# Performance work log

Hardware: AMD Instinct MI355X
Metric: run time of the kernel (lower is better)

The kernel has to match this reference:

```python
import jax, jax.numpy as jnp
import numpy as np

N_NODES = 50000
N_EDGES = 1600000
D = 128        # fea_dim == hidden_units == dim_z
L = 3          # num_layers


def _gin_params(key, scale=0.05):
    ks = jax.random.split(key, 7)
    return dict(
        W1=jax.random.normal(ks[0], (L, D, D), jnp.float32) * scale,
        b1=jnp.zeros((L, D), jnp.float32),
        W2=jax.random.normal(ks[1], (L, D, D), jnp.float32) * scale,
        b2=jnp.zeros((L, D), jnp.float32),
        eps=jnp.zeros((L,), jnp.float32),
        Wout=jax.random.normal(ks[2], (D, D), jnp.float32) * scale,
        bout=jnp.zeros((D,), jnp.float32),
    )


def setup_inputs() -> dict:
    key = jax.random.key(0)
    k_x, k_s, k_d, k_m, k_sd = jax.random.split(key, 5)
    inp = {
        'x': jax.random.normal(k_x, (N_NODES, D), jnp.float32),
        'edge_src': jax.random.randint(k_s, (N_EDGES,), 0, N_NODES, jnp.int32),
        'edge_dst': jax.random.randint(k_d, (N_EDGES,), 0, N_NODES, jnp.int32),
    }
    for pref, k in (('mean_', k_m), ('std_', k_sd)):
        for name, v in _gin_params(k).items():
            inp[pref + name] = v
    inp['ln_gamma'] = jnp.ones((D,), jnp.float32)
    inp['ln_beta'] = jnp.zeros((D,), jnp.float32)
    return inp


def _gin(x, src, dst, W1, b1, W2, b2, eps, Wout, bout):
    # Standard GIN: h = MLP((1+eps)*h + sum_{j->i} h_j), Sigmoid activation
    h = x
    n = x.shape[0]
    for l in range(L):
        agg = jax.ops.segment_sum(h[src], dst, num_segments=n)  # [N, D]
        h = (1.0 + eps[l]) * h + agg
        h = jax.nn.sigmoid(h @ W1[l] + b1[l]) @ W2[l] + b2[l]
    return h @ Wout + bout  # [N, dim_z]


def _layernorm(v, g, b, eps=1e-5):
    m = jnp.mean(v, axis=-1, keepdims=True)
    var = jnp.var(v, axis=-1, keepdims=True)
    return (v - m) * jax.lax.rsqrt(var + eps) * g + b


def reference(x, edge_src, edge_dst,
              mean_W1, mean_b1, mean_W2, mean_b2, mean_eps, mean_Wout, mean_bout,
              std_W1, std_b1, std_W2, std_b2, std_eps, std_Wout, std_bout,
              ln_gamma, ln_beta):
    mean_v = _layernorm(_gin(x, edge_src, edge_dst, mean_W1, mean_b1, mean_W2,
                             mean_b2, mean_eps, mean_Wout, mean_bout),
                        ln_gamma, ln_beta)
    # NOTE: source applies bn_mean to the std path too (faithful to bug)
    std_v = _layernorm(_gin(x, edge_src, edge_dst, std_W1, std_b1, std_W2,
                            std_b2, std_eps, std_Wout, std_bout),
                       ln_gamma, ln_beta)
    epsilon = jax.random.normal(jax.random.key(42), mean_v.shape, mean_v.dtype)
    samples = mean_v + epsilon * std_v
    return (samples, mean_v, std_v)
```

## Files before the change

### kernel.cpp

```cpp
#include <hip/hip_runtime.h>
#include <math.h>

#define NNODES 50000
#define NEDGES 1600000
#define DIM    128
#define NHID   (NNODES * DIM)
#define TPB    256
#define NTILES ((NNODES + 63) / 64)

#define NBINS  196
#define BINSZ  256
#define EPT    16
#define CHUNK  (TPB * EPT)
#define NCHUNKS ((NEDGES + CHUNK - 1) / CHUNK)
#define BINCAP 10240

typedef unsigned short bf16_t;
typedef __attribute__((ext_vector_type(8))) short short8;
typedef __attribute__((ext_vector_type(4))) float f32x4;

__device__ __forceinline__ float bf_lo(unsigned u) { return __uint_as_float(u << 16); }
__device__ __forceinline__ float bf_hi(unsigned u) { return __uint_as_float(u & 0xFFFF0000u); }
__device__ __forceinline__ bf16_t f2bf(float f) {
    unsigned u = __float_as_uint(f);
    u += 0x7FFFu + ((u >> 16) & 1u);
    return (bf16_t)(u >> 16);
}
__device__ __forceinline__ unsigned pack2bf(float a, float b) {
    return (unsigned)f2bf(a) | ((unsigned)f2bf(b) << 16);
}

union S8U { short8 v; uint4 u4; unsigned us[4]; };

__global__ __launch_bounds__(TPB) void bin_hist_kernel(
    const int* __restrict__ dst, int* __restrict__ gcnt)
{
    __shared__ int lcnt[NBINS];
    const int tid = threadIdx.x;
    for (int i = tid; i < NBINS; i += TPB) lcnt[i] = 0;
    __syncthreads();
    const int base = blockIdx.x * CHUNK;
    #pragma unroll
    for (int k = 0; k < EPT; ++k) {
        int e = base + k * TPB + tid;
        if (e < NEDGES) atomicAdd(&lcnt[dst[e] >> 8], 1);
    }
    __syncthreads();
    for (int i = tid; i < NBINS; i += TPB) {
        int c = lcnt[i];
        if (c) atomicAdd(&gcnt[i], c);
    }
}

__global__ __launch_bounds__(64) void bin_scan_kernel(
    const int* __restrict__ gcnt, int* __restrict__ start, int* __restrict__ bcur,
    int* __restrict__ off)
{
    const int lane = threadIdx.x;
    int c[4];
    int s = 0;
    #pragma unroll
    for (int k = 0; k < 4; ++k) {
        int b = 4 * lane + k;
        c[k] = (b < NBINS) ? gcnt[b] : 0;
        s += c[k];
    }
    int incl = s;
    #pragma unroll
    for (int d = 1; d < 64; d <<= 1) {
        int t = __shfl_up(incl, d);
        if (lane >= d) incl += t;
    }
    int excl = incl - s;
    #pragma unroll
    for (int k = 0; k < 4; ++k) {
        int b = 4 * lane + k;
        if (b < NBINS) { start[b] = excl; bcur[b] = excl; }
        excl += c[k];
    }
    if (lane == 63) { start[NBINS] = excl; off[NNODES] = excl; }
}

__global__ __launch_bounds__(TPB) void bin_scatter_kernel(
    const int* __restrict__ src, const int* __restrict__ dst,
    int* __restrict__ bcur, unsigned* __restrict__ bucket)
{
    __shared__ int lcnt[NBINS];
    __shared__ int lcur[NBINS];
    const int tid = threadIdx.x;
    for (int i = tid; i < NBINS; i += TPB) lcnt[i] = 0;
    __syncthreads();

    unsigned pk[EPT];
    int bn[EPT];
    const int base = blockIdx.x * CHUNK;
    #pragma unroll
    for (int k = 0; k < EPT; ++k) {
        int e = base + k * TPB + tid;
        int b = -1; unsigned p = 0;
        if (e < NEDGES) {
            int d = dst[e];
            int s = src[e];
            b = d >> 8;
            p = ((unsigned)(d & 255) << 16) | (unsigned)s;
            atomicAdd(&lcnt[b], 1);
        }
        pk[k] = p; bn[k] = b;
    }
    __syncthreads();
    for (int i = tid; i < NBINS; i += TPB) {
        int c = lcnt[i];
        lcur[i] = (c > 0) ? atomicAdd(&bcur[i], c) : 0;
    }
    __syncthreads();
    #pragma unroll
    for (int k = 0; k < EPT; ++k) {
        if (bn[k] >= 0) {
            int p = atomicAdd(&lcur[bn[k]], 1);
            bucket[p] = pk[k];
        }
    }
}

__global__ __launch_bounds__(TPB) void build_csr_kernel(
    const int* __restrict__ start, unsigned* __restrict__ bucket,
    int* __restrict__ off)
{
    __shared__ unsigned se[BINCAP];
    __shared__ int lcnt[BINSZ];
    __shared__ int lofs[BINSZ];
    __shared__ int wsum[4];
    const int tid = threadIdx.x;
    const int b = blockIdx.x;
    const int j0 = start[b], j1 = start[b + 1];
    const int n = j1 - j0;

    lcnt[tid] = 0;
    for (int i = tid; i < n; i += TPB) se[i] = bucket[j0 + i];
    __syncthreads();
    for (int i = tid; i < n; i += TPB) atomicAdd(&lcnt[se[i] >> 16], 1);
    __syncthreads();

    const int lane = tid & 63, wid = tid >> 6;
    int v = lcnt[tid];
    int s = v;
    #pragma unroll
    for (int d = 1; d < 64; d <<= 1) {
        int t = __shfl_up(s, d);
        if (lane >= d) s += t;
    }
    if (lane == 63) wsum[wid] = s;
    __syncthreads();
    if (tid == 0) {
        int a = 0;
        #pragma unroll
        for (int k = 0; k < 4; ++k) { int t = wsum[k]; wsum[k] = a; a += t; }
    }
    __syncthreads();
    int excl = wsum[wid] + s - v;
    lofs[tid] = excl;
    int node = b * BINSZ + tid;
    if (node < NNODES) off[node] = j0 + excl;
    __syncthreads();

    for (int i = tid; i < n; i += TPB) {
        unsigned e = se[i];
        int pos = atomicAdd(&lofs[e >> 16], 1);
        bucket[j0 + pos] = e & 0xFFFFu;
    }
}

__global__ __launch_bounds__(TPB) void gather_agg_f32_kernel(
    const float* __restrict__ h, const int* __restrict__ off,
    const unsigned* __restrict__ bucket, float* __restrict__ acat)
{
    int node = blockIdx.x * (TPB / 64) + (threadIdx.x >> 6);
    int lane = threadIdx.x & 63;
    if (node >= NNODES) return;
    int j0 = off[node], j1 = off[node + 1];
    const float* base = h + 2 * lane;
    float ax = 0.0f, ay = 0.0f;
    int j = j0;
    for (; j + 8 <= j1; j += 8) {
        unsigned s[8];
        #pragma unroll
        for (int k = 0; k < 8; ++k) s[k] = bucket[j + k];
        float2 v[8];
        #pragma unroll
        for (int k = 0; k < 8; ++k) v[k] = *(const float2*)(base + (size_t)s[k] * DIM);
        #pragma unroll
        for (int k = 0; k < 8; ++k) { ax += v[k].x; ay += v[k].y; }
    }
    for (; j < j1; ++j) {
        float2 v0 = *(const float2*)(base + (size_t)bucket[j] * DIM);
        ax += v0.x; ay += v0.y;
    }
    *(float2*)(acat + (size_t)node * 256 + 2 * lane) = make_float2(ax, ay);
}

__global__ __launch_bounds__(TPB) void gather_cat_kernel(
    const bf16_t* __restrict__ hc, const int* __restrict__ off,
    const unsigned* __restrict__ bucket, float* __restrict__ acat)
{
    int node = blockIdx.x * (TPB / 64) + (threadIdx.x >> 6);
    int lane = threadIdx.x & 63;
    if (node >= NNODES) return;
    int j0 = off[node], j1 = off[node + 1];
    const unsigned* base = (const unsigned*)hc;
    float ax = 0.f, ay = 0.f, bx = 0.f, by = 0.f;
    int j = j0;
    for (; j + 8 <= j1; j += 8) {
        unsigned s[8];
        #pragma unroll
        for (int k = 0; k < 8; ++k) s[k] = bucket[j + k];
        unsigned um[8], uv[8];
        #pragma unroll
        for (int k = 0; k < 8; ++k) {
            const unsigned* rp = base + (size_t)s[k] * 128;
            um[k] = rp[lane];
            uv[k] = rp[64 + lane];
        }
        #pragma unroll
        for (int k = 0; k < 8; ++k) {
            ax += bf_lo(um[k]); ay += bf_hi(um[k]);
            bx += bf_lo(uv[k]); by += bf_hi(uv[k]);
        }
    }
    for (; j < j1; ++j) {
        const unsigned* rp = base + (size_t)bucket[j] * 128;
        unsigned um = rp[lane], uv = rp[64 + lane];
        ax += bf_lo(um); ay += bf_hi(um);
        bx += bf_lo(uv); by += bf_hi(uv);
    }
    float* ar = acat + (size_t)node * 256;
    *(float2*)(ar + 2 * lane)       = make_float2(ax, ay);
    *(float2*)(ar + 128 + 2 * lane) = make_float2(bx, by);
}

template <class HinT, int INSTRIDE>
__global__ __launch_bounds__(TPB, 2) void fused_layer_kernel(
    const HinT* __restrict__ hin, const float* __restrict__ acat, int aggByPath,
    const float* __restrict__ eps0, const float* __restrict__ eps1, int eps_idx,
    const float* __restrict__ W1_0, const float* __restrict__ b1_0,
    const float* __restrict__ W2_0, const float* __restrict__ b2_0,
    const float* __restrict__ W1_1, const float* __restrict__ b1_1,
    const float* __restrict__ W2_1, const float* __restrict__ b2_1,
    bf16_t* __restrict__ out)
{
    __shared__ short sW1t[128 * 136];
    __shared__ short sW2t[128 * 136];
    float* y1buf = (float*)sW1t;

    const int p = (blockIdx.x >= NTILES) ? 1 : 0;
    const int t = blockIdx.x - p * NTILES;
    const float* W1 = p ? W1_1 : W1_0;
    const float* b1 = p ? b1_1 : b1_0;
    const float* W2 = p ? W2_1 : W2_0;
    const float* b2 = p ? b2_1 : b2_0;
    const float* epsp = p ? eps1 : eps0;
    const HinT* hbase = (INSTRIDE == 256) ? (hin + p * 128) : hin;
    const float* abase = acat + (aggByPath ? p * 128 : 0);
    bf16_t* ob = out + p * 128;

    const int tid = threadIdx.x;
    #pragma unroll
    for (int it = 0; it < 8; ++it) {
        int idx = it * 256 + tid;
        int n = idx & 127, koct = idx >> 7;
        float f1[8], f2[8];
        #pragma unroll
        for (int j = 0; j < 8; ++j) {
            f1[j] = W1[(8 * koct + j) * 128 + n];
            f2[j] = W2[(8 * koct + j) * 128 + n];
        }
        uint4 u1, u2;
        u1.x = pack2bf(f1[0], f1[1]); u1.y = pack2bf(f1[2], f1[3]);
        u1.z = pack2bf(f1[4], f1[5]); u1.w = pack2bf(f1[6], f1[7]);
        u2.x = pack2bf(f2[0], f2[1]); u2.y = pack2bf(f2[2], f2[3]);
        u2.z = pack2bf(f2[4], f2[5]); u2.w = pack2bf(f2[6], f2[7]);
        *(uint4*)&sW1t[n * 136 + 8 * koct] = u1;
        *(uint4*)&sW2t[n * 136 + 8 * koct] = u2;
    }
    __syncthreads();

    const int lane = tid & 63, w = tid >> 6;
    const int m = lane & 15, quad = lane >> 4;

    short8 bf1[32];
    #pragma unroll
    for (int c = 0; c < 8; ++c)
        #pragma unroll
        for (int k0 = 0; k0 < 4; ++k0)
            bf1[c * 4 + k0] = *(const short8*)&sW1t[(16 * c + m) * 136 + 32 * k0 + 8 * quad];
    __syncthreads();

    const float scale = 1.0f + epsp[eps_idx];
    float b1v[8], b2v[8];
    #pragma unroll
    for (int c = 0; c < 8; ++c) { b1v[c] = b1[16 * c + m]; b2v[c] = b2[16 * c + m]; }

    const int arow = min(t * 64 + 16 * w + m, NNODES - 1);

    short8 afh[4], afl[4];
    #pragma unroll
    for (int k0 = 0; k0 < 4; ++k0) {
        const int kb = 32 * k0 + 8 * quad;
        float zf[8];
        if constexpr (sizeof(HinT) == 4) {
            const float* hp = (const float*)hbase + (size_t)arow * INSTRIDE + kb;
            float4 h0 = *(const float4*)hp;
            float4 h1 = *(const float4*)(hp + 4);
            zf[0] = h0.x; zf[1] = h0.y; zf[2] = h0.z; zf[3] = h0.w;
            zf[4] = h1.x; zf[5] = h1.y; zf[6] = h1.z; zf[7] = h1.w;
        } else {
            uint4 hu = *(const uint4*)((const bf16_t*)hbase + (size_t)arow * INSTRIDE + kb);
            zf[0] = bf_lo(hu.x); zf[1] = bf_hi(hu.x);
            zf[2] = bf_lo(hu.y); zf[3] = bf_hi(hu.y);
            zf[4] = bf_lo(hu.z); zf[5] = bf_hi(hu.z);
            zf[6] = bf_lo(hu.w); zf[7] = bf_hi(hu.w);
        }
        const float* ap = abase + (size_t)arow * 256 + kb;
        float4 a0 = *(const float4*)ap;
        float4 a1 = *(const float4*)(ap + 4);
        zf[0] = fmaf(scale, zf[0], a0.x); zf[1] = fmaf(scale, zf[1], a0.y);
        zf[2] = fmaf(scale, zf[2], a0.z); zf[3] = fmaf(scale, zf[3], a0.w);
        zf[4] = fmaf(scale, zf[4], a1.x); zf[5] = fmaf(scale, zf[5], a1.y);
        zf[6] = fmaf(scale, zf[6], a1.z); zf[7] = fmaf(scale, zf[7], a1.w);
        S8U hi;
        hi.us[0] = pack2bf(zf[0], zf[1]); hi.us[1] = pack2bf(zf[2], zf[3]);
        hi.us[2] = pack2bf(zf[4], zf[5]); hi.us[3] = pack2bf(zf[6], zf[7]);
        afh[k0] = hi.v;
        S8U lo;
        float lw[8];
        lw[0] = zf[0] - bf_lo(hi.us[0]); lw[1] = zf[1] - bf_hi(hi.us[0]);
        lw[2] = zf[2] - bf_lo(hi.us[1]); lw[3] = zf[3] - bf_hi(hi.us[1]);
        lw[4] = zf[4] - bf_lo(hi.us[2]); lw[5] = zf[5] - bf_hi(hi.us[2]);
        lw[6] = zf[6] - bf_lo(hi.us[3]); lw[7] = zf[7] - bf_hi(hi.us[3]);
        lo.us[0] = pack2bf(lw[0], lw[1]); lo.us[1] = pack2bf(lw[2], lw[3]);
        lo.us[2] = pack2bf(lw[4], lw[5]); lo.us[3] = pack2bf(lw[6], lw[7]);
        afl[k0] = lo.v;
    }

    f32x4 acc[8];
    #pragma unroll
    for (int c = 0; c < 8; ++c) acc[c] = (f32x4){0.f, 0.f, 0.f, 0.f};
    #pragma unroll
    for (int k0 = 0; k0 < 4; ++k0) {
        #pragma unroll
        for (int c = 0; c < 8; ++c)
            acc[c] = __builtin_amdgcn_mfma_f32_16x16x32_bf16(
                afl[k0], bf1[c * 4 + k0], acc[c], 0, 0, 0);
        #pragma unroll
        for (int c = 0; c < 8; ++c)
            acc[c] = __builtin_amdgcn_mfma_f32_16x16x32_bf16(
                afh[k0], bf1[c * 4 + k0], acc[c], 0, 0, 0);
    }

    const int rloc0 = 16 * w + 4 * quad;
    #pragma unroll
    for (int r = 0; r < 4; ++r) {
        #pragma unroll
        for (int c = 0; c < 8; ++c) {
            float y = acc[c][r] + b1v[c];
            y = 1.0f / (1.0f + expf(-y));
            y1buf[(rloc0 + r) * 132 + 16 * c + m] = y;
        }
    }
    __syncthreads();

    f32x4 acc2[8];
    #pragma unroll
    for (int c = 0; c < 8; ++c) acc2[c] = (f32x4){0.f, 0.f, 0.f, 0.f};
    #pragma unroll
    for (int k0 = 0; k0 < 4; ++k0) {
        const int kb = 32 * k0 + 8 * quad;
        const float* yp = &y1buf[(16 * w + m) * 132 + kb];
        float4 p0 = *(const float4*)yp;
        float4 p1 = *(const float4*)(yp + 4);
        S8U a2;
        a2.us[0] = pack2bf(p0.x, p0.y); a2.us[1] = pack2bf(p0.z, p0.w);
        a2.us[2] = pack2bf(p1.x, p1.y); a2.us[3] = pack2bf(p1.z, p1.w);
        #pragma unroll
        for (int c = 0; c < 8; ++c) {
            short8 b2f = *(const short8*)&sW2t[(16 * c + m) * 136 + kb];
            acc2[c] = __builtin_amdgcn_mfma_f32_16x16x32_bf16(
                a2.v, b2f, acc2[c], 0, 0, 0);
        }
    }

    const int row0 = t * 64 + 16 * w + 4 * quad;
    #pragma unroll
    for (int r = 0; r < 4; ++r) {
        const int grow = row0 + r;
        if (grow < NNODES) {
            bf16_t* op = ob + (size_t)grow * 256 + m;
            #pragma unroll
            for (int c = 0; c < 8; ++c) op[16 * c] = f2bf(acc2[c][r] + b2v[c]);
        }
    }
}

__global__ __launch_bounds__(TPB) void final_proj_kernel(
    const bf16_t* __restrict__ hc,
    const float* __restrict__ Wo0, const float* __restrict__ bo0,
    const float* __restrict__ Wo1, const float* __restrict__ bo1,
    const float* __restrict__ gamma, const float* __restrict__ beta,
    float* __restrict__ M, float* __restrict__ V)
{
    __shared__ short sWt[128 * 136];

    const int p = (blockIdx.x >= NTILES) ? 1 : 0;
    const int t = blockIdx.x - p * NTILES;
    const float* W = p ? Wo1 : Wo0;
    const float* bias = p ? bo1 : bo0;
    const bf16_t* hbase = hc + p * 128;
    float* out = p ? V : M;

    const int tid = threadIdx.x;
    #pragma unroll
    for (int it = 0; it < 8; ++it) {
        int idx = it * 256 + tid;
        int n = idx & 127, koct = idx >> 7;
        float f[8];
        #pragma unroll
        for (int j = 0; j < 8; ++j) f[j] = W[(8 * koct + j) * 128 + n];
        uint4 u;
        u.x = pack2bf(f[0], f[1]); u.y = pack2bf(f[2], f[3]);
        u.z = pack2bf(f[4], f[5]); u.w = pack2bf(f[6], f[7]);
        *(uint4*)&sWt[n * 136 + 8 * koct] = u;
    }
    __syncthreads();

    const int lane = tid & 63, w = tid >> 6;
    const int m = lane & 15, quad = lane >> 4;

    short8 bf[32];
    #pragma unroll
    for (int c = 0; c < 8; ++c)
        #pragma unroll
        for (int k0 = 0; k0 < 4; ++k0)
            bf[c * 4 + k0] = *(const short8*)&sWt[(16 * c + m) * 136 + 32 * k0 + 8 * quad];

    float bias_v[8], g_v[8], bt_v[8];
    #pragma unroll
    for (int c = 0; c < 8; ++c) {
        bias_v[c] = bias[16 * c + m];
        g_v[c] = gamma[16 * c + m];
        bt_v[c] = beta[16 * c + m];
    }

    const int arow = min(t * 64 + 16 * w + m, NNODES - 1);
    short8 af[4];
    #pragma unroll
    for (int k0 = 0; k0 < 4; ++k0)
        af[k0] = *(const short8*)(hbase + (size_t)arow * 256 + 32 * k0 + 8 * quad);

    f32x4 acc[8];
    #pragma unroll
    for (int c = 0; c < 8; ++c) acc[c] = (f32x4){0.f, 0.f, 0.f, 0.f};
    #pragma unroll
    for (int k0 = 0; k0 < 4; ++k0)
        #pragma unroll
        for (int c = 0; c < 8; ++c)
            acc[c] = __builtin_amdgcn_mfma_f32_16x16x32_bf16(
                af[k0], bf[c * 4 + k0], acc[c], 0, 0, 0);

    const int row0 = t * 64 + 16 * w + 4 * quad;
    #pragma unroll
    for (int r = 0; r < 4; ++r) {
        const int grow = row0 + r;
        float y[8];
        #pragma unroll
        for (int c = 0; c < 8; ++c) y[c] = acc[c][r] + bias_v[c];
        float s1 = 0.f, s2 = 0.f;
        #pragma unroll
        for (int c = 0; c < 8; ++c) { s1 += y[c]; s2 = fmaf(y[c], y[c], s2); }
        #pragma unroll
        for (int d = 1; d < 16; d <<= 1) {
            s1 += __shfl_xor(s1, d);
            s2 += __shfl_xor(s2, d);
        }
        float mean = s1 * (1.0f / DIM);
        float var  = s2 * (1.0f / DIM) - mean * mean;
        float rstd = rsqrtf(var + 1e-5f);
        if (grow < NNODES) {
            float* op = out + (size_t)grow * DIM + m;
            #pragma unroll
            for (int c = 0; c < 8; ++c)
                op[16 * c] = fmaf((y[c] - mean) * rstd, g_v[c], bt_v[c]);
        }
    }
}

__device__ __forceinline__ unsigned rotl32(unsigned x, int r) {
    return (x << r) | (x >> (32 - r));
}

__device__ __forceinline__ unsigned threefry_xor(unsigned c0, unsigned c1) {
    const unsigned k0 = 0u, k1 = 42u;
    const unsigned k2 = k0 ^ k1 ^ 0x1BD11BDAu;
    unsigned x0 = c0 + k0;
    unsigned x1 = c1 + k1;
#define TF_ROUND(R) { x0 += x1; x1 = rotl32(x1, R); x1 ^= x0; }
    TF_ROUND(13) TF_ROUND(15) TF_ROUND(26) TF_ROUND(6)
    x0 += k1; x1 += k2 + 1u;
    TF_ROUND(17) TF_ROUND(29) TF_ROUND(16) TF_ROUND(24)
    x0 += k2; x1 += k0 + 2u;
    TF_ROUND(13) TF_ROUND(15) TF_ROUND(26) TF_ROUND(6)
    x0 += k0; x1 += k1 + 3u;
    TF_ROUND(17) TF_ROUND(29) TF_ROUND(16) TF_ROUND(24)
    x0 += k1; x1 += k2 + 4u;
    TF_ROUND(13) TF_ROUND(15) TF_ROUND(26) TF_ROUND(6)
    x0 += k2; x1 += k0 + 5u;
#undef TF_ROUND
    return x0 ^ x1;
}

__device__ __forceinline__ float bits_to_normal(unsigned bits) {
    float f = __uint_as_float((bits >> 9) | 0x3F800000u) - 1.0f;
    const float lo = -0.99999994f;
    float u = __fadd_rn(__fmul_rn(f, 2.0f), lo);
    u = fmaxf(lo, u);
    float w = -log1pf(-(u * u));
    float p;
    if (w < 5.0f) {
        w -= 2.5f;
        p = 2.81022636e-08f;
        p = fmaf(p, w, 3.43273939e-07f);
        p = fmaf(p, w, -3.5233877e-06f);
        p = fmaf(p, w, -4.39150654e-06f);
        p = fmaf(p, w, 0.00021858087f);
        p = fmaf(p, w, -0.00125372503f);
        p = fmaf(p, w, -0.00417768164f);
        p = fmaf(p, w, 0.246640727f);
        p = fmaf(p, w, 1.50140941f);
    } else {
        w = sqrtf(w) - 3.0f;
        p = -0.000200214257f;
        p = fmaf(p, w, 0.000100950558f);
        p = fmaf(p, w, 0.00134934322f);
        p = fmaf(p, w, -0.00367342844f);
        p = fmaf(p, w, 0.00573950773f);
        p = fmaf(p, w, -0.0076224613f);
        p = fmaf(p, w, 0.00943887047f);
        p = fmaf(p, w, 1.00167406f);
        p = fmaf(p, w, 2.83297682f);
    }
    return 1.41421356f * (p * u);
}

__global__ __launch_bounds__(TPB) void samples_kernel(
    const float* __restrict__ mean_v, const float* __restrict__ std_v,
    float* __restrict__ samples)
{
    int t = blockIdx.x * TPB + threadIdx.x;
    if (t >= NHID / 4) return;
    float4 m = ((const float4*)mean_v)[t];
    float4 s = ((const float4*)std_v)[t];
    float e[4];
    #pragma unroll
    for (int q = 0; q < 4; q++) {
        unsigned i = 4u * (unsigned)t + (unsigned)q;
        e[q] = bits_to_normal(threefry_xor(0u, i));
    }
    float4 r;
    r.x = fmaf(e[0], s.x, m.x);
    r.y = fmaf(e[1], s.y, m.y);
    r.z = fmaf(e[2], s.z, m.z);
    r.w = fmaf(e[3], s.w, m.w);
    ((float4*)samples)[t] = r;
}

extern "C" void kernel_launch(void* const* d_in, const int* in_sizes, int n_in,
                              void* d_out, int out_size, void* d_ws, size_t ws_size,
                              hipStream_t stream)
{
    const float* x     = (const float*)d_in[0];
    const int*   esrc  = (const int*)d_in[1];
    const int*   edst  = (const int*)d_in[2];
    const float* prm[2][7];
    for (int p = 0; p < 2; p++)
        for (int i = 0; i < 7; i++)
            prm[p][i] = (const float*)d_in[3 + p * 7 + i];
    const float* gamma = (const float*)d_in[17];
    const float* beta  = (const float*)d_in[18];

    float*  S  = (float*)d_out;
    float*  M  = S + NHID;
    float*  V  = M + NHID;
    bf16_t* Hc = (bf16_t*)S;
    float*  ACAT = M;

    int* gcnt  = (int*)d_ws;
    int* start = gcnt + NBINS;
    int* bcur  = start + NBINS + 1;
    int* off   = bcur + NBINS;
    unsigned* bucket = (unsigned*)(off + NNODES + 1);

    const dim3 gChunk(NCHUNKS);
    const dim3 gBin(NBINS);
    const dim3 gGather((NNODES + (TPB / 64) - 1) / (TPB / 64));
    const dim3 gTile2(2 * NTILES);
    const dim3 gSamp((NHID / 4 + TPB - 1) / TPB);

    hipMemsetAsync(gcnt, 0, NBINS * sizeof(int), stream);
    bin_hist_kernel<<<gChunk, TPB, 0, stream>>>(edst, gcnt);
    bin_scan_kernel<<<1, 64, 0, stream>>>(gcnt, start, bcur, off);
    bin_scatter_kernel<<<gChunk, TPB, 0, stream>>>(esrc, edst, bcur, bucket);
    build_csr_kernel<<<gBin, TPB, 0, stream>>>(start, bucket, off);

    gather_agg_f32_kernel<<<gGather, TPB, 0, stream>>>(x, off, bucket, ACAT);

    fused_layer_kernel<float, DIM><<<gTile2, TPB, 0, stream>>>(
        x, ACAT, 0, prm[0][4], prm[1][4], 0,
        prm[0][0], prm[0][1], prm[0][2], prm[0][3],
        prm[1][0], prm[1][1], prm[1][2], prm[1][3], Hc);

    for (int l = 1; l < 3; l++) {
        gather_cat_kernel<<<gGather, TPB, 0, stream>>>(Hc, off, bucket, ACAT);
        fused_layer_kernel<bf16_t, 256><<<gTile2, TPB, 0, stream>>>(
            Hc, ACAT, 1, prm[0][4], prm[1][4], l,
            prm[0][0] + (size_t)l * DIM * DIM, prm[0][1] + l * DIM,
            prm[0][2] + (size_t)l * DIM * DIM, prm[0][3] + l * DIM,
            prm[1][0] + (size_t)l * DIM * DIM, prm[1][1] + l * DIM,
            prm[1][2] + (size_t)l * DIM * DIM, prm[1][3] + l * DIM, Hc);
    }

    final_proj_kernel<<<gTile2, TPB, 0, stream>>>(
        Hc, prm[0][5], prm[0][6], prm[1][5], prm[1][6], gamma, beta, M, V);

    samples_kernel<<<gSamp, TPB, 0, stream>>>(M, V, S);
}
```

Baseline: 671.3 us.

## Fuse final projection, layernorm and sampling; widen gather unroll and vector loads

Merges the final projection/layernorm kernel with the sampling kernel, so each tile computes both paths and writes samples directly, without re-reading the mean and std outputs or paying an extra launch. The gather kernels add a 16-edge unrolled loop to keep more loads in flight, and the bf16 gather uses one 8-byte load per lane plus a float4 store instead of two 4-byte loads. The fused kernel uses more registers and shared memory per block and launches half as many blocks.

```diff
diff --git a/kernel.cpp b/kernel.cpp
--- a/kernel.cpp
+++ b/kernel.cpp
@@ -181,6 +181,16 @@
     const float* base = h + 2 * lane;
     float ax = 0.0f, ay = 0.0f;
     int j = j0;
+    for (; j + 16 <= j1; j += 16) {
+        unsigned s[16];
+        #pragma unroll
+        for (int k = 0; k < 16; ++k) s[k] = bucket[j + k];
+        float2 v[16];
+        #pragma unroll
+        for (int k = 0; k < 16; ++k) v[k] = *(const float2*)(base + (size_t)s[k] * DIM);
+        #pragma unroll
+        for (int k = 0; k < 16; ++k) { ax += v[k].x; ay += v[k].y; }
+    }
     for (; j + 8 <= j1; j += 8) {
         unsigned s[8];
         #pragma unroll
@@ -206,35 +216,41 @@
     int lane = threadIdx.x & 63;
     if (node >= NNODES) return;
     int j0 = off[node], j1 = off[node + 1];
-    const unsigned* base = (const unsigned*)hc;
-    float ax = 0.f, ay = 0.f, bx = 0.f, by = 0.f;
+    const uint2* base = (const uint2*)hc + lane;
+    float a0 = 0.f, a1 = 0.f, a2 = 0.f, a3 = 0.f;
     int j = j0;
+    for (; j + 16 <= j1; j += 16) {
+        unsigned s[16];
+        #pragma unroll
+        for (int k = 0; k < 16; ++k) s[k] = bucket[j + k];
+        uint2 u[16];
+        #pragma unroll
+        for (int k = 0; k < 16; ++k) u[k] = base[(size_t)s[k] * 64];
+        #pragma unroll
+        for (int k = 0; k < 16; ++k) {
+            a0 += bf_lo(u[k].x); a1 += bf_hi(u[k].x);
+            a2 += bf_lo(u[k].y); a3 += bf_hi(u[k].y);
+        }
+    }
     for (; j + 8 <= j1; j += 8) {
         unsigned s[8];
         #pragma unroll
         for (int k = 0; k < 8; ++k) s[k] = bucket[j + k];
-        unsigned um[8], uv[8];
+        uint2 u[8];
+        #pragma unroll
+        for (int k = 0; k < 8; ++k) u[k] = base[(size_t)s[k] * 64];
         #pragma unroll
         for (int k = 0; k < 8; ++k) {
-            const unsigned* rp = base + (size_t)s[k] * 128;
-            um[k] = rp[lane];
-            uv[k] = rp[64 + lane];
-        }
-        #pragma unroll
-        for (int k = 0; k < 8; ++k) {
-            ax += bf_lo(um[k]); ay += bf_hi(um[k]);
-            bx += bf_lo(uv[k]); by += bf_hi(uv[k]);
+            a0 += bf_lo(u[k].x); a1 += bf_hi(u[k].x);
+            a2 += bf_lo(u[k].y); a3 += bf_hi(u[k].y);
         }
     }
     for (; j < j1; ++j) {
-        const unsigned* rp = base + (size_t)bucket[j] * 128;
-        unsigned um = rp[lane], uv = rp[64 + lane];
-        ax += bf_lo(um); ay += bf_hi(um);
-        bx += bf_lo(uv); by += bf_hi(uv);
-    }
-    float* ar = acat + (size_t)node * 256;
-    *(float2*)(ar + 2 * lane)       = make_float2(ax, ay);
-    *(float2*)(ar + 128 + 2 * lane) = make_float2(bx, by);
+        uint2 u = base[(size_t)bucket[j] * 64];
+        a0 += bf_lo(u.x); a1 += bf_hi(u.x);
+        a2 += bf_lo(u.y); a3 += bf_hi(u.y);
+    }
+    *(float4*)(acat + (size_t)node * 256 + 4 * lane) = make_float4(a0, a1, a2, a3);
 }
 
 template <class HinT, int INSTRIDE>
@@ -396,98 +412,6 @@
             bf16_t* op = ob + (size_t)grow * 256 + m;
             #pragma unroll
             for (int c = 0; c < 8; ++c) op[16 * c] = f2bf(acc2[c][r] + b2v[c]);
-        }
-    }
-}
-
-__global__ __launch_bounds__(TPB) void final_proj_kernel(
-    const bf16_t* __restrict__ hc,
-    const float* __restrict__ Wo0, const float* __restrict__ bo0,
-    const float* __restrict__ Wo1, const float* __restrict__ bo1,
-    const float* __restrict__ gamma, const float* __restrict__ beta,
-    float* __restrict__ M, float* __restrict__ V)
-{
-    __shared__ short sWt[128 * 136];
-
-    const int p = (blockIdx.x >= NTILES) ? 1 : 0;
-    const int t = blockIdx.x - p * NTILES;
-    const float* W = p ? Wo1 : Wo0;
-    const float* bias = p ? bo1 : bo0;
-    const bf16_t* hbase = hc + p * 128;
-    float* out = p ? V : M;
-
-    const int tid = threadIdx.x;
-    #pragma unroll
-    for (int it = 0; it < 8; ++it) {
-        int idx = it * 256 + tid;
-        int n = idx & 127, koct = idx >> 7;
-        float f[8];
-        #pragma unroll
-        for (int j = 0; j < 8; ++j) f[j] = W[(8 * koct + j) * 128 + n];
-        uint4 u;
-        u.x = pack2bf(f[0], f[1]); u.y = pack2bf(f[2], f[3]);
-        u.z = pack2bf(f[4], f[5]); u.w = pack2bf(f[6], f[7]);
-        *(uint4*)&sWt[n * 136 + 8 * koct] = u;
-    }
-    __syncthreads();
-
-    const int lane = tid & 63, w = tid >> 6;
-    const int m = lane & 15, quad = lane >> 4;
-
-    short8 bf[32];
-    #pragma unroll
-    for (int c = 0; c < 8; ++c)
-        #pragma unroll
-        for (int k0 = 0; k0 < 4; ++k0)
-            bf[c * 4 + k0] = *(const short8*)&sWt[(16 * c + m) * 136 + 32 * k0 + 8 * quad];
-
-    float bias_v[8], g_v[8], bt_v[8];
-    #pragma unroll
-    for (int c = 0; c < 8; ++c) {
-        bias_v[c] = bias[16 * c + m];
-        g_v[c] = gamma[16 * c + m];
-        bt_v[c] = beta[16 * c + m];
-    }
-
-    const int arow = min(t * 64 + 16 * w + m, NNODES - 1);
-    short8 af[4];
-    #pragma unroll
-    for (int k0 = 0; k0 < 4; ++k0)
-        af[k0] = *(const short8*)(hbase + (size_t)arow * 256 + 32 * k0 + 8 * quad);
-
-    f32x4 acc[8];
-    #pragma unroll
-    for (int c = 0; c < 8; ++c) acc[c] = (f32x4){0.f, 0.f, 0.f, 0.f};
-    #pragma unroll
-    for (int k0 = 0; k0 < 4; ++k0)
-        #pragma unroll
-        for (int c = 0; c < 8; ++c)
-            acc[c] = __builtin_amdgcn_mfma_f32_16x16x32_bf16(
-                af[k0], bf[c * 4 + k0], acc[c], 0, 0, 0);
-
-    const int row0 = t * 64 + 16 * w + 4 * quad;
-    #pragma unroll
-    for (int r = 0; r < 4; ++r) {
-        const int grow = row0 + r;
-        float y[8];
-        #pragma unroll
-        for (int c = 0; c < 8; ++c) y[c] = acc[c][r] + bias_v[c];
-        float s1 = 0.f, s2 = 0.f;
-        #pragma unroll
-        for (int c = 0; c < 8; ++c) { s1 += y[c]; s2 = fmaf(y[c], y[c], s2); }
-        #pragma unroll
-        for (int d = 1; d < 16; d <<= 1) {
-            s1 += __shfl_xor(s1, d);
-            s2 += __shfl_xor(s2, d);
-        }
-        float mean = s1 * (1.0f / DIM);
-        float var  = s2 * (1.0f / DIM) - mean * mean;
-        float rstd = rsqrtf(var + 1e-5f);
-        if (grow < NNODES) {
-            float* op = out + (size_t)grow * DIM + m;
-            #pragma unroll
-            for (int c = 0; c < 8; ++c)
-                op[16 * c] = fmaf((y[c] - mean) * rstd, g_v[c], bt_v[c]);
         }
     }
 }
@@ -549,26 +473,142 @@
     return 1.41421356f * (p * u);
 }
 
-__global__ __launch_bounds__(TPB) void samples_kernel(
-    const float* __restrict__ mean_v, const float* __restrict__ std_v,
-    float* __restrict__ samples)
-{
-    int t = blockIdx.x * TPB + threadIdx.x;
-    if (t >= NHID / 4) return;
-    float4 m = ((const float4*)mean_v)[t];
-    float4 s = ((const float4*)std_v)[t];
-    float e[4];
-    #pragma unroll
-    for (int q = 0; q < 4; q++) {
-        unsigned i = 4u * (unsigned)t + (unsigned)q;
-        e[q] = bits_to_normal(threefry_xor(0u, i));
-    }
-    float4 r;
-    r.x = fmaf(e[0], s.x, m.x);
-    r.y = fmaf(e[1], s.y, m.y);
-    r.z = fmaf(e[2], s.z, m.z);
-    r.w = fmaf(e[3], s.w, m.w);
-    ((float4*)samples)[t] = r;
+__global__ __launch_bounds__(TPB) void final_samples_kernel(
+    const bf16_t* __restrict__ hc,
+    const float* __restrict__ Wo0, const float* __restrict__ bo0,
+    const float* __restrict__ Wo1, const float* __restrict__ bo1,
+    const float* __restrict__ gamma, const float* __restrict__ beta,
+    float* __restrict__ S, float* __restrict__ M, float* __restrict__ V)
+{
+    __shared__ short sW0[128 * 136];
+    __shared__ short sW1[128 * 136];
+
+    const int tid = threadIdx.x;
+    #pragma unroll
+    for (int it = 0; it < 8; ++it) {
+        int idx = it * 256 + tid;
+        int n = idx & 127, koct = idx >> 7;
+        float f0[8], f1[8];
+        #pragma unroll
+        for (int j = 0; j < 8; ++j) {
+            f0[j] = Wo0[(8 * koct + j) * 128 + n];
+            f1[j] = Wo1[(8 * koct + j) * 128 + n];
+        }
+        uint4 u0, u1;
+        u0.x = pack2bf(f0[0], f0[1]); u0.y = pack2bf(f0[2], f0[3]);
+        u0.z = pack2bf(f0[4], f0[5]); u0.w = pack2bf(f0[6], f0[7]);
+        u1.x = pack2bf(f1[0], f1[1]); u1.y = pack2bf(f1[2], f1[3]);
+        u1.z = pack2bf(f1[4], f1[5]); u1.w = pack2bf(f1[6], f1[7]);
+        *(uint4*)&sW0[n * 136 + 8 * koct] = u0;
+        *(uint4*)&sW1[n * 136 + 8 * koct] = u1;
+    }
+    __syncthreads();
+
+    const int lane = tid & 63, w = tid >> 6;
+    const int m = lane & 15, quad = lane >> 4;
+    const int t = blockIdx.x;
+    const int arow = min(t * 64 + 16 * w + m, NNODES - 1);
+
+    short8 af0[4], af1[4];
+    #pragma unroll
+    for (int k0 = 0; k0 < 4; ++k0) {
+        const bf16_t* hp = hc + (size_t)arow * 256 + 32 * k0 + 8 * quad;
+        af0[k0] = *(const short8*)hp;
+        af1[k0] = *(const short8*)(hp + 128);
+    }
+    __syncthreads();
+
+    float g_v[8], bt_v[8], bias0[8], bias1[8];
+    #pragma unroll
+    for (int c = 0; c < 8; ++c) {
+        g_v[c] = gamma[16 * c + m];
+        bt_v[c] = beta[16 * c + m];
+        bias0[c] = bo0[16 * c + m];
+        bias1[c] = bo1[16 * c + m];
+    }
+
+    const int row0 = t * 64 + 16 * w + 4 * quad;
+    float y0[4][8], y1[4][8];
+
+    {
+        f32x4 acc[8];
+        #pragma unroll
+        for (int c = 0; c < 8; ++c) acc[c] = (f32x4){0.f, 0.f, 0.f, 0.f};
+        #pragma unroll
+        for (int k0 = 0; k0 < 4; ++k0) {
+            const int kb = 32 * k0 + 8 * quad;
+            #pragma unroll
+            for (int c = 0; c < 8; ++c)
+                acc[c] = __builtin_amdgcn_mfma_f32_16x16x32_bf16(
+                    af0[k0], *(const short8*)&sW0[(16 * c + m) * 136 + kb], acc[c], 0, 0, 0);
+        }
+        #pragma unroll
+        for (int r = 0; r < 4; ++r) {
+            float y[8];
+            #pragma unroll
+            for (int c = 0; c < 8; ++c) y[c] = acc[c][r] + bias0[c];
+            float s1 = 0.f, s2 = 0.f;
+            #pragma unroll
+            for (int c = 0; c < 8; ++c) { s1 += y[c]; s2 = fmaf(y[c], y[c], s2); }
+            #pragma unroll
+            for (int d = 1; d < 16; d <<= 1) { s1 += __shfl_xor(s1, d); s2 += __shfl_xor(s2, d); }
+            float mean = s1 * (1.0f / DIM);
+            float var  = s2 * (1.0f / DIM) - mean * mean;
+            float rstd = rsqrtf(var + 1e-5f);
+            #pragma unroll
+            for (int c = 0; c < 8; ++c)
+                y0[r][c] = fmaf((y[c] - mean) * rstd, g_v[c], bt_v[c]);
+        }
+    }
+    {
+        f32x4 acc[8];
+        #pragma unroll
+        for (int c = 0; c < 8; ++c) acc[c] = (f32x4){0.f, 0.f, 0.f, 0.f};
+        #pragma unroll
+        for (int k0 = 0; k0 < 4; ++k0) {
+            const int kb = 32 * k0 + 8 * quad;
+            #pragma unroll
+            for (int c = 0; c < 8; ++c)
+                acc[c] = __builtin_amdgcn_mfma_f32_16x16x32_bf16(
+                    af1[k0], *(const short8*)&sW1[(16 * c + m) * 136 + kb], acc[c], 0, 0, 0);
+        }
+        #pragma unroll
+        for (int r = 0; r < 4; ++r) {
+            float y[8];
+            #pragma unroll
+            for (int c = 0; c < 8; ++c) y[c] = acc[c][r] + bias1[c];
+            float s1 = 0.f, s2 = 0.f;
+            #pragma unroll
+            for (int c = 0; c < 8; ++c) { s1 += y[c]; s2 = fmaf(y[c], y[c], s2); }
+            #pragma unroll
+            for (int d = 1; d < 16; d <<= 1) { s1 += __shfl_xor(s1, d); s2 += __shfl_xor(s2, d); }
+            float mean = s1 * (1.0f / DIM);
+            float var  = s2 * (1.0f / DIM) - mean * mean;
+            float rstd = rsqrtf(var + 1e-5f);
+            #pragma unroll
+            for (int c = 0; c < 8; ++c)
+                y1[r][c] = fmaf((y[c] - mean) * rstd, g_v[c], bt_v[c]);
+        }
+    }
+
+    #pragma unroll
+    for (int r = 0; r < 4; ++r) {
+        const int grow = row0 + r;
+        if (grow < NNODES) {
+            float* mp = M + (size_t)grow * DIM + m;
+            float* vp = V + (size_t)grow * DIM + m;
+            float* sp = S + (size_t)grow * DIM + m;
+            #pragma unroll
+            for (int c = 0; c < 8; ++c) {
+                float mv = y0[r][c], sv = y1[r][c];
+                mp[16 * c] = mv;
+                vp[16 * c] = sv;
+                unsigned i = (unsigned)grow * 128u + (unsigned)(16 * c + m);
+                float e = bits_to_normal(threefry_xor(0u, i));
+                sp[16 * c] = fmaf(e, sv, mv);
+            }
+        }
+    }
 }
 
 extern "C" void kernel_launch(void* const* d_in, const int* in_sizes, int n_in,
@@ -601,7 +641,7 @@
     const dim3 gBin(NBINS);
     const dim3 gGather((NNODES + (TPB / 64) - 1) / (TPB / 64));
     const dim3 gTile2(2 * NTILES);
-    const dim3 gSamp((NHID / 4 + TPB - 1) / TPB);
+    const dim3 gTile(NTILES);
 
     hipMemsetAsync(gcnt, 0, NBINS * sizeof(int), stream);
     bin_hist_kernel<<<gChunk, TPB, 0, stream>>>(edst, gcnt);
@@ -626,8 +666,6 @@
             prm[1][2] + (size_t)l * DIM * DIM, prm[1][3] + l * DIM, Hc);
     }
 
-    final_proj_kernel<<<gTile2, TPB, 0, stream>>>(
-        Hc, prm[0][5], prm[0][6], prm[1][5], prm[1][6], gamma, beta, M, V);
-
-    samples_kernel<<<gSamp, TPB, 0, stream>>>(M, V, S);
-}
+    final_samples_kernel<<<gTile, TPB, 0, stream>>>(
+        Hc, prm[0][5], prm[0][6], prm[1][5], prm[1][6], gamma, beta, S, M, V);
+}
```

Measured after the change: 698.5 us. +4.1%, slower.

## Cut fused layer LDS and registers for higher occupancy; widen gather loads

Applied to the files above, without the earlier changes.

The fused GIN layer kernel now keeps one bf16 weight buffer in LDS, loading W1 first and then reloading W2 into the same buffer after the first GEMM. It stores the sigmoid output as bf16 in a separate smaller buffer and reads W1 fragments from LDS inside the MFMA loop instead of holding 32 fragments in registers. Launch bounds rise from 2 to 4 blocks per SM to use the smaller LDS and register footprint. Separately, both gather kernels gain a 16-wide unrolled loop, and the concatenated bf16 gather switches to one 8-byte load per lane plus a single float4 store. The cost is an extra barrier and serialized W2 staging per block, more LDS reads in the inner loop, and bf16 rounding of the intermediate written to LDS instead of converting it on read.

```diff
diff --git a/kernel.cpp b/kernel.cpp
--- a/kernel.cpp
+++ b/kernel.cpp
@@ -181,6 +181,16 @@
     const float* base = h + 2 * lane;
     float ax = 0.0f, ay = 0.0f;
     int j = j0;
+    for (; j + 16 <= j1; j += 16) {
+        unsigned s[16];
+        #pragma unroll
+        for (int k = 0; k < 16; ++k) s[k] = bucket[j + k];
+        float2 v[16];
+        #pragma unroll
+        for (int k = 0; k < 16; ++k) v[k] = *(const float2*)(base + (size_t)s[k] * DIM);
+        #pragma unroll
+        for (int k = 0; k < 16; ++k) { ax += v[k].x; ay += v[k].y; }
+    }
     for (; j + 8 <= j1; j += 8) {
         unsigned s[8];
         #pragma unroll
@@ -206,39 +216,45 @@
     int lane = threadIdx.x & 63;
     if (node >= NNODES) return;
     int j0 = off[node], j1 = off[node + 1];
-    const unsigned* base = (const unsigned*)hc;
-    float ax = 0.f, ay = 0.f, bx = 0.f, by = 0.f;
+    const uint2* base = (const uint2*)hc + lane;
+    float a0 = 0.f, a1 = 0.f, a2 = 0.f, a3 = 0.f;
     int j = j0;
+    for (; j + 16 <= j1; j += 16) {
+        unsigned s[16];
+        #pragma unroll
+        for (int k = 0; k < 16; ++k) s[k] = bucket[j + k];
+        uint2 u[16];
+        #pragma unroll
+        for (int k = 0; k < 16; ++k) u[k] = base[(size_t)s[k] * 64];
+        #pragma unroll
+        for (int k = 0; k < 16; ++k) {
+            a0 += bf_lo(u[k].x); a1 += bf_hi(u[k].x);
+            a2 += bf_lo(u[k].y); a3 += bf_hi(u[k].y);
+        }
+    }
     for (; j + 8 <= j1; j += 8) {
         unsigned s[8];
         #pragma unroll
         for (int k = 0; k < 8; ++k) s[k] = bucket[j + k];
-        unsigned um[8], uv[8];
+        uint2 u[8];
+        #pragma unroll
+        for (int k = 0; k < 8; ++k) u[k] = base[(size_t)s[k] * 64];
         #pragma unroll
         for (int k = 0; k < 8; ++k) {
-            const unsigned* rp = base + (size_t)s[k] * 128;
-            um[k] = rp[lane];
-            uv[k] = rp[64 + lane];
-        }
-        #pragma unroll
-        for (int k = 0; k < 8; ++k) {
-            ax += bf_lo(um[k]); ay += bf_hi(um[k]);
-            bx += bf_lo(uv[k]); by += bf_hi(uv[k]);
+            a0 += bf_lo(u[k].x); a1 += bf_hi(u[k].x);
+            a2 += bf_lo(u[k].y); a3 += bf_hi(u[k].y);
         }
     }
     for (; j < j1; ++j) {
-        const unsigned* rp = base + (size_t)bucket[j] * 128;
-        unsigned um = rp[lane], uv = rp[64 + lane];
-        ax += bf_lo(um); ay += bf_hi(um);
-        bx += bf_lo(uv); by += bf_hi(uv);
-    }
-    float* ar = acat + (size_t)node * 256;
-    *(float2*)(ar + 2 * lane)       = make_float2(ax, ay);
-    *(float2*)(ar + 128 + 2 * lane) = make_float2(bx, by);
+        uint2 u = base[(size_t)bucket[j] * 64];
+        a0 += bf_lo(u.x); a1 += bf_hi(u.x);
+        a2 += bf_lo(u.y); a3 += bf_hi(u.y);
+    }
+    *(float4*)(acat + (size_t)node * 256 + 4 * lane) = make_float4(a0, a1, a2, a3);
 }
 
 template <class HinT, int INSTRIDE>
-__global__ __launch_bounds__(TPB, 2) void fused_layer_kernel(
+__global__ __launch_bounds__(TPB, 4) void fused_layer_kernel(
     const HinT* __restrict__ hin, const float* __restrict__ acat, int aggByPath,
     const float* __restrict__ eps0, const float* __restrict__ eps1, int eps_idx,
     const float* __restrict__ W1_0, const float* __restrict__ b1_0,
@@ -247,9 +263,8 @@
     const float* __restrict__ W2_1, const float* __restrict__ b2_1,
     bf16_t* __restrict__ out)
 {
-    __shared__ short sW1t[128 * 136];
-    __shared__ short sW2t[128 * 136];
-    float* y1buf = (float*)sW1t;
+    __shared__ short sWt[128 * 136];
+    __shared__ short y1b[64 * 136];
 
     const int p = (blockIdx.x >= NTILES) ? 1 : 0;
     const int t = blockIdx.x - p * NTILES;
@@ -267,32 +282,18 @@
     for (int it = 0; it < 8; ++it) {
         int idx = it * 256 + tid;
         int n = idx & 127, koct = idx >> 7;
-        float f1[8], f2[8];
-        #pragma unroll
-        for (int j = 0; j < 8; ++j) {
-            f1[j] = W1[(8 * koct + j) * 128 + n];
-            f2[j] = W2[(8 * koct + j) * 128 + n];
-        }
-        uint4 u1, u2;
+        float f1[8];
+        #pragma unroll
+        for (int j = 0; j < 8; ++j) f1[j] = W1[(8 * koct + j) * 128 + n];
+        uint4 u1;
         u1.x = pack2bf(f1[0], f1[1]); u1.y = pack2bf(f1[2], f1[3]);
         u1.z = pack2bf(f1[4], f1[5]); u1.w = pack2bf(f1[6], f1[7]);
-        u2.x = pack2bf(f2[0], f2[1]); u2.y = pack2bf(f2[2], f2[3]);
-        u2.z = pack2bf(f2[4], f2[5]); u2.w = pack2bf(f2[6], f2[7]);
-        *(uint4*)&sW1t[n * 136 + 8 * koct] = u1;
-        *(uint4*)&sW2t[n * 136 + 8 * koct] = u2;
+        *(uint4*)&sWt[n * 136 + 8 * koct] = u1;
     }
     __syncthreads();
 
     const int lane = tid & 63, w = tid >> 6;
     const int m = lane & 15, quad = lane >> 4;
-
-    short8 bf1[32];
-    #pragma unroll
-    for (int c = 0; c < 8; ++c)
-        #pragma unroll
-        for (int k0 = 0; k0 < 4; ++k0)
-            bf1[c * 4 + k0] = *(const short8*)&sW1t[(16 * c + m) * 136 + 32 * k0 + 8 * quad];
-    __syncthreads();
 
     const float scale = 1.0f + epsp[eps_idx];
     float b1v[8], b2v[8];
@@ -346,14 +347,13 @@
     for (int c = 0; c < 8; ++c) acc[c] = (f32x4){0.f, 0.f, 0.f, 0.f};
     #pragma unroll
     for (int k0 = 0; k0 < 4; ++k0) {
-        #pragma unroll
-        for (int c = 0; c < 8; ++c)
-            acc[c] = __builtin_amdgcn_mfma_f32_16x16x32_bf16(
-                afl[k0], bf1[c * 4 + k0], acc[c], 0, 0, 0);
-        #pragma unroll
-        for (int c = 0; c < 8; ++c)
-            acc[c] = __builtin_amdgcn_mfma_f32_16x16x32_bf16(
-                afh[k0], bf1[c * 4 + k0], acc[c], 0, 0, 0);
+        const int kb = 32 * k0 + 8 * quad;
+        #pragma unroll
+        for (int c = 0; c < 8; ++c) {
+            short8 bfr = *(const short8*)&sWt[(16 * c + m) * 136 + kb];
+            acc[c] = __builtin_amdgcn_mfma_f32_16x16x32_bf16(afl[k0], bfr, acc[c], 0, 0, 0);
+            acc[c] = __builtin_amdgcn_mfma_f32_16x16x32_bf16(afh[k0], bfr, acc[c], 0, 0, 0);
+        }
     }
 
     const int rloc0 = 16 * w + 4 * quad;
@@ -363,8 +363,22 @@
         for (int c = 0; c < 8; ++c) {
             float y = acc[c][r] + b1v[c];
             y = 1.0f / (1.0f + expf(-y));
-            y1buf[(rloc0 + r) * 132 + 16 * c + m] = y;
-        }
+            y1b[(rloc0 + r) * 136 + 16 * c + m] = (short)f2bf(y);
+        }
+    }
+    __syncthreads();
+
+    #pragma unroll
+    for (int it = 0; it < 8; ++it) {
+        int idx = it * 256 + tid;
+        int n = idx & 127, koct = idx >> 7;
+        float f2[8];
+        #pragma unroll
+        for (int j = 0; j < 8; ++j) f2[j] = W2[(8 * koct + j) * 128 + n];
+        uint4 u2;
+        u2.x = pack2bf(f2[0], f2[1]); u2.y = pack2bf(f2[2], f2[3]);
+        u2.z = pack2bf(f2[4], f2[5]); u2.w = pack2bf(f2[6], f2[7]);
+        *(uint4*)&sWt[n * 136 + 8 * koct] = u2;
     }
     __syncthreads();
 
@@ -374,17 +388,11 @@
     #pragma unroll
     for (int k0 = 0; k0 < 4; ++k0) {
         const int kb = 32 * k0 + 8 * quad;
-        const float* yp = &y1buf[(16 * w + m) * 132 + kb];
-        float4 p0 = *(const float4*)yp;
-        float4 p1 = *(const float4*)(yp + 4);
-        S8U a2;
-        a2.us[0] = pack2bf(p0.x, p0.y); a2.us[1] = pack2bf(p0.z, p0.w);
-        a2.us[2] = pack2bf(p1.x, p1.y); a2.us[3] = pack2bf(p1.z, p1.w);
+        short8 a2 = *(const short8*)&y1b[(16 * w + m) * 136 + kb];
         #pragma unroll
         for (int c = 0; c < 8; ++c) {
-            short8 b2f = *(const short8*)&sW2t[(16 * c + m) * 136 + kb];
-            acc2[c] = __builtin_amdgcn_mfma_f32_16x16x32_bf16(
-                a2.v, b2f, acc2[c], 0, 0, 0);
+            short8 b2f = *(const short8*)&sWt[(16 * c + m) * 136 + kb];
+            acc2[c] = __builtin_amdgcn_mfma_f32_16x16x32_bf16(a2, b2f, acc2[c], 0, 0, 0);
         }
     }
 
```

Result: faster. 644.2 us (-4.0%).
